# Performance work log

Measured on AMD Instinct MI355X. Metric: run time of the kernel, lower is better.

The kernel has to match this reference:

```python
import jax, jax.numpy as jnp
import numpy as np

B, C, H, W = 16384, 1, 2048, 1
HID = 5


def setup_inputs() -> dict:
    key = jax.random.key(0)
    kx, kl, k1, k2, k3, k4 = jax.random.split(key, 6)
    x = jax.random.normal(kx, (B, C, H, W), dtype=jnp.float32)
    # random ragged lengths in [1, H]; zero out padded tail so the module's
    # (x != 0).any(dim=2) mask recovers exactly these lengths
    lengths = jax.random.randint(kl, (B,), 1, H + 1)
    t_idx = jnp.arange(H)
    valid = (t_idx[None, :] < lengths[:, None])  # [B, H]
    x = x * valid[:, None, :, None].astype(jnp.float32)
    s = 1.0 / np.sqrt(HID)
    W_ih = jax.random.uniform(k1, (4 * HID, 1), minval=-s, maxval=s, dtype=jnp.float32)
    W_hh = jax.random.uniform(k2, (4 * HID, HID), minval=-s, maxval=s, dtype=jnp.float32)
    b_ih = jax.random.uniform(k3, (4 * HID,), minval=-s, maxval=s, dtype=jnp.float32)
    b_hh = jax.random.uniform(k4, (4 * HID,), minval=-s, maxval=s, dtype=jnp.float32)
    return {"x": x, "W_ih": W_ih, "W_hh": W_hh, "b_ih": b_ih, "b_hh": b_hh}


def reference(x, W_ih, W_hh, b_ih, b_hh):
    b, c, h, w = x.shape
    feats = c * w  # == 1 (LSTM input_size)
    xr = x.reshape(b, h, feats)  # [B, T, 1]
    mask = jnp.any(xr != 0, axis=2)  # [B, T]
    lengths = mask.sum(axis=1).astype(jnp.int32)  # [B]

    bias = b_ih + b_hh  # [4H]
    # precompute input projection for all timesteps: [B, T, 4H]
    x_proj = jnp.einsum('btf,gf->btg', xr, W_ih) + bias
    xs = jnp.moveaxis(x_proj, 1, 0)  # [T, B, 4H]

    h0 = jnp.zeros((b, HID), dtype=x.dtype)
    c0 = jnp.zeros((b, HID), dtype=x.dtype)

    def step(carry, inp):
        hp, cp = carry
        xg, t = inp
        gates = xg + hp @ W_hh.T  # [B, 4H]
        i, f, g, o = jnp.split(gates, 4, axis=1)
        i = jax.nn.sigmoid(i)
        f = jax.nn.sigmoid(f)
        g = jnp.tanh(g)
        o = jax.nn.sigmoid(o)
        cn = f * cp + i * g
        hn = o * jnp.tanh(cn)
        # packed semantics: only advance state while t < length (per sample)
        upd = (t < lengths)[:, None]
        hn = jnp.where(upd, hn, hp)
        cn = jnp.where(upd, cn, cp)
        return (hn, cn), None

    (hT, cT), _ = jax.lax.scan(step, (h0, c0), (xs, jnp.arange(h)))
    return hT[None]  # [1, B, HID] matching torch h shape
```

## Files before the change

### kernel.cpp

```cpp
#include <hip/hip_runtime.h>

#define Bn    16384
#define Tn    2048
#define HIDn  5
#define NBINS 2048

typedef float v2f __attribute__((ext_vector_type(2)));

static __device__ __forceinline__ float rcp_fast(float v) {
    return __builtin_amdgcn_rcpf(v);
}
static __device__ __forceinline__ float exp2_fast(float v) {
    return __builtin_amdgcn_exp2f(v);
}

template <int K>
static __device__ __forceinline__ float bcast8(float v) {
    return __int_as_float(
        __builtin_amdgcn_ds_swizzle(__float_as_int(v), (K << 5) | 0x18));
}

__global__ void zero_kernel(int* __restrict__ gbins) {
    gbins[blockIdx.x * 256 + threadIdx.x] = 0;
}

__global__ __launch_bounds__(256) void len_kernel(const float* __restrict__ x,
                                                  int* __restrict__ lengths,
                                                  int* __restrict__ gbins) {
    const int gtid = blockIdx.x * 256 + threadIdx.x;
    const int row  = gtid >> 6;
    const int lane = threadIdx.x & 63;
    const float4* r = reinterpret_cast<const float4*>(x + (size_t)row * Tn);
    int cnt = 0;
    #pragma unroll
    for (int i = 0; i < Tn / 4 / 64; ++i) {
        float4 v = r[i * 64 + lane];
        cnt += (v.x != 0.0f) + (v.y != 0.0f) + (v.z != 0.0f) + (v.w != 0.0f);
    }
    #pragma unroll
    for (int off = 32; off > 0; off >>= 1) cnt += __shfl_xor(cnt, off, 64);
    if (lane == 0) {
        lengths[row] = cnt;
        const int d = max(0, min(NBINS - 1, NBINS - cnt));
        atomicAdd(&gbins[d], 1);
    }
}

__global__ __launch_bounds__(1024) void sort_kernel(const int* __restrict__ lengths,
                                                    const int* __restrict__ gbins,
                                                    int* __restrict__ perm) {
    __shared__ int bins[NBINS];
    __shared__ int bsum[1024];
    const int tid = threadIdx.x;
    bins[tid]        = gbins[tid];
    bins[tid + 1024] = gbins[tid + 1024];
    __syncthreads();
    const int a0 = bins[2 * tid], a1 = bins[2 * tid + 1];
    const int s = a0 + a1;
    bsum[tid] = s;
    __syncthreads();
    int acc = s;
    for (int off = 1; off < 1024; off <<= 1) {
        int v = (tid >= off) ? bsum[tid - off] : 0;
        __syncthreads();
        acc += v;
        bsum[tid] = acc;
        __syncthreads();
    }
    const int excl = acc - s;
    bins[2 * tid]     = excl;
    bins[2 * tid + 1] = excl + a0;
    __syncthreads();
    for (int i = tid; i < Bn; i += 1024) {
        int d = NBINS - lengths[i];
        d = max(0, min(NBINS - 1, d));
        const int p = atomicAdd(&bins[d], 1);
        perm[p] = i;
    }
}

__global__ __launch_bounds__(256, 2) void lstm_kernel(const float* __restrict__ x,
                                                      const float* __restrict__ Wih,
                                                      const float* __restrict__ Whh,
                                                      const float* __restrict__ bih,
                                                      const float* __restrict__ bhh,
                                                      const int* __restrict__ lengths,
                                                      const int* __restrict__ perm,
                                                      float* __restrict__ out) {
    const int gtid = blockIdx.x * 256 + threadIdx.x;
    const int grp  = gtid >> 3;
    const int lsub = threadIdx.x & 7;
    const int k    = min(lsub, 4);

    if ((blockIdx.x >> 8) & 1) __builtin_amdgcn_s_setprio(1);

    const int b   = perm[grp];
    const int len = lengths[b];

    const float S1 = -1.4426950408889634f;
    const float S2 = 2.0f * S1;
    v2f wihA, wihB, bA, bB, whhA[HIDn], whhB[HIDn];
    {
        const int gi = k, gf = 5 + k, gg = 10 + k, go = 15 + k;
        wihA = (v2f){ Wih[gi] * S1, Wih[gf] * S1 };
        wihB = (v2f){ Wih[gg] * S2, Wih[go] * S1 };
        bA   = (v2f){ (bih[gi] + bhh[gi]) * S1, (bih[gf] + bhh[gf]) * S1 };
        bB   = (v2f){ (bih[gg] + bhh[gg]) * S2, (bih[go] + bhh[go]) * S1 };
        #pragma unroll
        for (int kk = 0; kk < HIDn; ++kk) {
            whhA[kk] = (v2f){ Whh[gi * HIDn + kk] * S1, Whh[gf * HIDn + kk] * S1 };
            whhB[kk] = (v2f){ Whh[gg * HIDn + kk] * S2, Whh[go * HIDn + kk] * S1 };
        }
    }

    const float* xrow = x + (size_t)b * Tn;
    float h0 = 0, h1 = 0, h2 = 0, h3 = 0, h4 = 0;
    float hq = 0, c = 0;

    float4 xq = *reinterpret_cast<const float4*>(xrow);
    for (int t = 0; __any(t < len); t += 4) {
        const float4 xn = *reinterpret_cast<const float4*>(xrow + min(t + 4, Tn - 4));
        const float xs[4] = { xq.x, xq.y, xq.z, xq.w };
        #pragma unroll
        for (int s = 0; s < 4; ++s) {
            const float xv = xs[s];
            v2f pA = xv * wihA + bA;
            v2f pB = xv * wihB + bB;
            pA = h0 * whhA[0] + pA;  pB = h0 * whhB[0] + pB;
            pA = h1 * whhA[1] + pA;  pB = h1 * whhB[1] + pB;
            pA = h2 * whhA[2] + pA;  pB = h2 * whhB[2] + pB;
            pA = h3 * whhA[3] + pA;  pB = h3 * whhB[3] + pB;
            pA = h4 * whhA[4] + pA;  pB = h4 * whhB[4] + pB;
            const float eI = exp2_fast(pA.x);
            const float eF = exp2_fast(pA.y);
            const float eG = exp2_fast(pB.x);
            const float eO = exp2_fast(pB.y);
            const float gi_ = rcp_fast(1.0f + eI);
            const float gf_ = rcp_fast(1.0f + eF);
            const float rg  = rcp_fast(1.0f + eG);
            const float oo  = rcp_fast(1.0f + eO);
            const float tg  = fmaf(2.0f, rg, -1.0f);

            const float cn = fmaf(gf_, c, gi_ * tg);

            const float ec  = exp2_fast(cn * S2);
            const float rc  = rcp_fast(1.0f + ec);
            const float oo2 = oo + oo;
            const float hn  = fmaf(oo2, rc, -oo);

            const bool upd = (t + s) < len;
            c  = upd ? cn : c;
            hq = upd ? hn : hq;

            h0 = bcast8<0>(hq);
            h1 = bcast8<1>(hq);
            h2 = bcast8<2>(hq);
            h3 = bcast8<3>(hq);
            h4 = bcast8<4>(hq);
        }
        xq = xn;
    }

    if (lsub < HIDn) out[(size_t)b * HIDn + lsub] = hq;
}

extern "C" void kernel_launch(void* const* d_in, const int* in_sizes, int n_in,
                              void* d_out, int out_size, void* d_ws, size_t ws_size,
                              hipStream_t stream) {
    const float* x   = (const float*)d_in[0];
    const float* Wih = (const float*)d_in[1];
    const float* Whh = (const float*)d_in[2];
    const float* bih = (const float*)d_in[3];
    const float* bhh = (const float*)d_in[4];
    float* out = (float*)d_out;

    int* lengths = (int*)d_ws;
    int* perm    = lengths + Bn;
    int* gbins   = perm + Bn;

    zero_kernel<<<NBINS / 256, 256, 0, stream>>>(gbins);
    len_kernel<<<Bn / 4, 256, 0, stream>>>(x, lengths, gbins);
    sort_kernel<<<1, 1024, 0, stream>>>(lengths, gbins, perm);
    lstm_kernel<<<Bn * 8 / 256, 256, 0, stream>>>(x, Wih, Whh, bih, bhh,
                                                  lengths, perm, out);
}
```

Before: 577.8 us.

## Replace cell tanh with clamped odd polynomial and reassociate gate dot products

The tanh(c) exp2/rcp pair on the serial recurrence chain is replaced by a degree-27 odd Chebyshev-fit polynomial, evaluated Estrin-style on c clamped to [-4,4]. Its coefficients are computed on the host and passed as a kernel argument. The recurrent gate dot product is reassociated into a shallower tree, and the per-step masked select is dropped: the output is written at the step equal to len-1 instead. This shortens the dependency chain per timestep at the cost of extra FMAs, a small tanh approximation error, and a per-step compare and store branch.

Measured after the change: 653.6 us. 13.1% more time.

```diff
diff --git a/kernel.cpp b/kernel.cpp
--- a/kernel.cpp
+++ b/kernel.cpp
@@ -1,4 +1,5 @@
 #include <hip/hip_runtime.h>
+#include <cmath>
 
 #define Bn    16384
 #define Tn    2048
@@ -13,12 +14,20 @@
 static __device__ __forceinline__ float exp2_fast(float v) {
     return __builtin_amdgcn_exp2f(v);
 }
+static __device__ __forceinline__ float med3(float x, float lo, float hi) {
+    return __builtin_amdgcn_fmed3f(x, lo, hi);
+}
 
 template <int K>
 static __device__ __forceinline__ float bcast8(float v) {
     return __int_as_float(
         __builtin_amdgcn_ds_swizzle(__float_as_int(v), (K << 5) | 0x18));
 }
+
+struct SpineC {
+    float p0, p1, p2, p3, p4, p5, p6;
+    float p7, p8, p9, p10, p11, p12, p13;
+};
 
 __global__ void zero_kernel(int* __restrict__ gbins) {
     gbins[blockIdx.x * 256 + threadIdx.x] = 0;
@@ -86,7 +95,8 @@
                                                       const float* __restrict__ bhh,
                                                       const int* __restrict__ lengths,
                                                       const int* __restrict__ perm,
-                                                      float* __restrict__ out) {
+                                                      float* __restrict__ out,
+                                                      SpineC SC) {
     const int gtid = blockIdx.x * 256 + threadIdx.x;
     const int grp  = gtid >> 3;
     const int lsub = threadIdx.x & 7;
@@ -94,8 +104,9 @@
 
     if ((blockIdx.x >> 8) & 1) __builtin_amdgcn_s_setprio(1);
 
-    const int b   = perm[grp];
-    const int len = lengths[b];
+    const int b     = perm[grp];
+    const int len   = lengths[b];
+    const int mstep = max(len, 1) - 1;
 
     const float S1 = -1.4426950408889634f;
     const float S2 = 2.0f * S1;
@@ -115,7 +126,7 @@
 
     const float* xrow = x + (size_t)b * Tn;
     float h0 = 0, h1 = 0, h2 = 0, h3 = 0, h4 = 0;
-    float hq = 0, c = 0;
+    float c = 0;
 
     float4 xq = *reinterpret_cast<const float4*>(xrow);
     for (int t = 0; __any(t < len); t += 4) {
@@ -124,13 +135,21 @@
         #pragma unroll
         for (int s = 0; s < 4; ++s) {
             const float xv = xs[s];
-            v2f pA = xv * wihA + bA;
-            v2f pB = xv * wihB + bB;
-            pA = h0 * whhA[0] + pA;  pB = h0 * whhB[0] + pB;
-            pA = h1 * whhA[1] + pA;  pB = h1 * whhB[1] + pB;
-            pA = h2 * whhA[2] + pA;  pB = h2 * whhB[2] + pB;
-            pA = h3 * whhA[3] + pA;  pB = h3 * whhB[3] + pB;
-            pA = h4 * whhA[4] + pA;  pB = h4 * whhB[4] + pB;
+            const v2f xA = xv * wihA + bA;
+            const v2f xB = xv * wihB + bB;
+            const v2f tA0 = h0 * whhA[0] + xA;
+            const v2f tB0 = h0 * whhB[0] + xB;
+            const v2f mA2 = h2 * whhA[2];
+            const v2f mB2 = h2 * whhB[2];
+            const v2f tA1 = h1 * whhA[1] + mA2;
+            const v2f tB1 = h1 * whhB[1] + mB2;
+            const v2f mA4 = h4 * whhA[4];
+            const v2f mB4 = h4 * whhB[4];
+            const v2f tA2 = h3 * whhA[3] + mA4;
+            const v2f tB2 = h3 * whhB[3] + mB4;
+            const v2f pA = (tA0 + tA1) + tA2;
+            const v2f pB = (tB0 + tB1) + tB2;
+
             const float eI = exp2_fast(pA.x);
             const float eF = exp2_fast(pA.y);
             const float eG = exp2_fast(pB.x);
@@ -143,25 +162,61 @@
 
             const float cn = fmaf(gf_, c, gi_ * tg);
 
-            const float ec  = exp2_fast(cn * S2);
-            const float rc  = rcp_fast(1.0f + ec);
-            const float oo2 = oo + oo;
-            const float hn  = fmaf(oo2, rc, -oo);
-
-            const bool upd = (t + s) < len;
-            c  = upd ? cn : c;
-            hq = upd ? hn : hq;
-
-            h0 = bcast8<0>(hq);
-            h1 = bcast8<1>(hq);
-            h2 = bcast8<2>(hq);
-            h3 = bcast8<3>(hq);
-            h4 = bcast8<4>(hq);
+            const float cc = med3(cn, -4.0f, 4.0f);
+            const float u  = cc * cc;
+            const float A0 = fmaf(u, SC.p1,  SC.p0);
+            const float A1 = fmaf(u, SC.p3,  SC.p2);
+            const float A2 = fmaf(u, SC.p5,  SC.p4);
+            const float A3 = fmaf(u, SC.p7,  SC.p6);
+            const float A4 = fmaf(u, SC.p9,  SC.p8);
+            const float A5 = fmaf(u, SC.p11, SC.p10);
+            const float A6 = fmaf(u, SC.p13, SC.p12);
+            const float u2 = u * u, u4 = u2 * u2, u8 = u4 * u4;
+            const float B0 = fmaf(u2, A1, A0);
+            const float B1 = fmaf(u2, A3, A2);
+            const float B2 = fmaf(u2, A5, A4);
+            const float D0 = fmaf(u4, B1, B0);
+            const float D1 = fmaf(u4, A6, B2);
+            const float Pc = fmaf(u8, D1, D0);
+            const float hn = (cc * Pc) * oo;
+
+            if (lsub < HIDn && (t + s) == mstep)
+                out[(size_t)b * HIDn + lsub] = hn;
+            c = cn;
+
+            h0 = bcast8<0>(hn);
+            h1 = bcast8<1>(hn);
+            h2 = bcast8<2>(hn);
+            h3 = bcast8<3>(hn);
+            h4 = bcast8<4>(hn);
         }
         xq = xn;
     }
-
-    if (lsub < HIDn) out[(size_t)b * HIDn + lsub] = hq;
+}
+
+static void tanh_base_poly(int N, double* c) {
+    double yj[16], fj[16];
+    for (int j = 0; j < N; ++j) {
+        const double v = cos(M_PI * (2 * j + 1) / (2.0 * N));
+        const double y = 0.5 + 0.5 * v;
+        const double xx = 4.0 * sqrt(y);
+        yj[j] = y;
+        fj[j] = tanh(xx) / xx;
+    }
+    for (int k = 1; k < N; ++k)
+        for (int j = N - 1; j >= k; --j)
+            fj[j] = (fj[j] - fj[j - 1]) / (yj[j] - yj[j - k]);
+    for (int i = 0; i < 16; ++i) c[i] = 0.0;
+    c[0] = fj[N - 1];
+    int deg = 0;
+    for (int j = N - 2; j >= 0; --j) {
+        for (int i = deg; i >= 0; --i) {
+            c[i + 1] += c[i];
+            c[i] = -yj[j] * c[i];
+        }
+        ++deg;
+        c[0] += fj[j];
+    }
 }
 
 extern "C" void kernel_launch(void* const* d_in, const int* in_sizes, int n_in,
@@ -178,9 +233,21 @@
     int* perm    = lengths + Bn;
     int* gbins   = perm + Bn;
 
+    SpineC SC;
+    {
+        double c14[16];
+        tanh_base_poly(14, c14);
+        float p[14];
+        for (int i = 0; i < 14; ++i) p[i] = (float)ldexp(c14[i], -4 * i);
+        SC.p0  = p[0];  SC.p1  = p[1];  SC.p2  = p[2];  SC.p3  = p[3];
+        SC.p4  = p[4];  SC.p5  = p[5];  SC.p6  = p[6];  SC.p7  = p[7];
+        SC.p8  = p[8];  SC.p9  = p[9];  SC.p10 = p[10]; SC.p11 = p[11];
+        SC.p12 = p[12]; SC.p13 = p[13];
+    }
+
     zero_kernel<<<NBINS / 256, 256, 0, stream>>>(gbins);
     len_kernel<<<Bn / 4, 256, 0, stream>>>(x, lengths, gbins);
     sort_kernel<<<1, 1024, 0, stream>>>(lengths, gbins, perm);
     lstm_kernel<<<Bn * 8 / 256, 256, 0, stream>>>(x, Wih, Whh, bih, bhh,
-                                                  lengths, perm, out);
-}
+                                                  lengths, perm, out, SC);
+}
```
